# Kernel tuning notes

Hardware: AMD Instinct MI355X
Metric: run time of the kernel (lower is better)

## Reference

```python
import jax, jax.numpy as jnp
import numpy as np

NPOINT = 1024
NSAMPLE = 32
EPS = 1e-5


def setup_inputs() -> dict:
    key = jax.random.key(0)
    ks = jax.random.split(key, 8)
    B, N, D = 16, 4096, 64
    xyz = jax.random.normal(ks[0], (B, N, 3), dtype=jnp.float32)
    points = jax.random.normal(ks[1], (B, N, D), dtype=jnp.float32)

    def mk(k, o, i):
        return (jax.random.normal(k, (o, i), dtype=jnp.float32) * 0.05,
                jnp.zeros((o,), jnp.float32),   # conv bias
                jnp.ones((o,), jnp.float32),    # bn gamma
                jnp.zeros((o,), jnp.float32))   # bn beta

    W0, b0, g0, be0 = mk(ks[2], 64, 67)
    W1, b1, g1, be1 = mk(ks[3], 64, 64)
    W2, b2, g2, be2 = mk(ks[4], 128, 64)
    return dict(xyz=xyz, points=points,
                W0=W0, b0=b0, g0=g0, be0=be0,
                W1=W1, b1=b1, g1=g1, be1=be1,
                W2=W2, b2=b2, g2=g2, be2=be2)


def _fps(xyz, npoint):
    # Sequential farthest point sampling. xyz: [B,N,3] -> idx [B,npoint] int32.
    B, N, _ = xyz.shape
    bidx = jnp.arange(B)

    def step(carry, _):
        distance, farthest = carry
        centroid = xyz[bidx, farthest][:, None, :]          # [B,1,3]
        d = jnp.sum((xyz - centroid) ** 2, -1)              # [B,N]
        distance = jnp.minimum(distance, d)
        new_far = jnp.argmax(distance, -1).astype(jnp.int32)
        return (distance, new_far), farthest

    init = (jnp.full((B, N), jnp.inf, dtype=xyz.dtype),
            jnp.full((B,), N // 2, dtype=jnp.int32))
    _, cents = jax.lax.scan(step, init, None, length=npoint)
    return cents.T                                          # [B, npoint]


def _gather(p, idx):
    # p: [B,N,C], idx: [B,...] -> [B,...,C]
    return jax.vmap(lambda a, i: a[i])(p, idx)


def reference(xyz, points, W0, b0, g0, be0, W1, b1, g1, be1, W2, b2, g2, be2):
    B, N, _ = xyz.shape
    fps_idx = _fps(xyz, NPOINT)                             # [B,M]
    new_xyz = _gather(xyz, fps_idx)                         # [B,M,3]

    # squared distances [B,M,N], then k smallest neighbors
    d = (jnp.sum(new_xyz ** 2, -1)[:, :, None]
         + jnp.sum(xyz ** 2, -1)[:, None, :]
         - 2.0 * jnp.einsum('bmc,bnc->bmn', new_xyz, xyz))
    _, idx = jax.lax.top_k(-d, NSAMPLE)                     # [B,M,K]

    grouped_xyz = _gather(xyz, idx)                         # [B,M,K,3]
    rel = grouped_xyz - new_xyz[:, :, None, :]
    grouped_feat = _gather(points, idx)                     # [B,M,K,D]
    g = jnp.concatenate([rel, grouped_feat], axis=-1)       # [B,M,K,3+D]

    # 1x1 conv + BatchNorm2d (training-mode batch stats) + ReLU
    for W, b, gm, bt in ((W0, b0, g0, be0), (W1, b1, g1, be1), (W2, b2, g2, be2)):
        x = jnp.einsum('bmkc,oc->bmko', g, W) + b
        mu = x.mean((0, 1, 2))
        var = x.var((0, 1, 2))
        g = jax.nn.relu(gm * (x - mu) * jax.lax.rsqrt(var + EPS) + bt)

    new_points = g.max(axis=2)                              # [B,M,C_out]
    return new_xyz, new_points, fps_idx
```

## Files before the change

### kernel.cpp

```cpp
#include <hip/hip_runtime.h>
#include <math.h>

#define B_ 16
#define N_ 4096
#define D_ 64
#define M_ 1024
#define K_ 32
#define RTOT (B_*M_*K_)
#define EPSF 1e-5f

#define WT0B_OFF  0
#define WT1B_OFF  3072
#define WT2B_OFF  5120
#define ST_OFF    9216
#define BN_OFF    9728
#define NXW_OFF   10240
#define KIDX_OFF  59392
#define PK_OFF    583680
#define Y0B_OFF   2680832
#define PTS4_OFF  Y0B_OFF
#define PBF_OFF   19458048
#define SB0_OFF   36235264
#define SB1_OFF   (SB0_OFF + 8192)
#define SB2_OFF   (SB1_OFF + 8192)
#define WS_FAST_BYTES ((unsigned long long)(SB2_OFF + 16384) * 4ull)

typedef __attribute__((ext_vector_type(8))) short bf16x8;
typedef __attribute__((ext_vector_type(4))) float f32x4;

__device__ inline unsigned bf16u(float x) {
    unsigned u = __float_as_uint(x);
    return (u + 0x7FFFu + ((u >> 16) & 1u)) >> 16;
}
__device__ inline float ubf(unsigned short h) {
    return __uint_as_float(((unsigned)h) << 16);
}

#define ROR_MIN(kvar, CTRL) do {                                                   \
    unsigned _lo = (unsigned)(kvar), _hi = (unsigned)((kvar) >> 32);               \
    unsigned _rl = (unsigned)__builtin_amdgcn_update_dpp((int)_lo, (int)_lo, CTRL, 0xF, 0xF, false); \
    unsigned _rh = (unsigned)__builtin_amdgcn_update_dpp((int)_hi, (int)_hi, CTRL, 0xF, 0xF, false); \
    unsigned long long _o = ((unsigned long long)_rh << 32) | _rl;                 \
    if (_o < (kvar)) (kvar) = _o;                                                  \
} while (0)

__global__ void prep_kernel(const float* __restrict__ W0, const float* __restrict__ W1,
                            const float* __restrict__ W2, const float* __restrict__ points,
                            float* __restrict__ ws, int fast) {
    int tid = threadIdx.x;
    int bx = blockIdx.x;
    if (bx >= 17) {
        unsigned short* pbf = (unsigned short*)(ws + PBF_OFF);
        size_t base = (size_t)(bx - 17) * 2048 + (size_t)tid * 8;
        const float4* s = (const float4*)(points + base);
        float4 f0 = s[0], f1 = s[1];
        uint4 u;
        u.x = bf16u(f0.x) | (bf16u(f0.y) << 16);
        u.y = bf16u(f0.z) | (bf16u(f0.w) << 16);
        u.z = bf16u(f1.x) | (bf16u(f1.y) << 16);
        u.w = bf16u(f1.z) | (bf16u(f1.w) << 16);
        *(uint4*)(pbf + base) = u;
        return;
    }
    if (bx > 0) {
        if (fast) {
            float* sb = ws + SB0_OFF + (bx - 1) * 2048;
            for (int i = tid; i < 2048; i += 256) sb[i] = 0.f;
        }
        return;
    }
    unsigned short* wt0b = (unsigned short*)(ws + WT0B_OFF);
    unsigned short* wt1b = (unsigned short*)(ws + WT1B_OFF);
    unsigned short* wt2b = (unsigned short*)(ws + WT2B_OFF);
    float* st = ws + ST_OFF;
    for (int i = tid; i < 512; i += 256) st[i] = 0.f;
    for (int i = tid; i < 64*96; i += 256) {
        int o = i / 96, k = i - o*96;
        float w = 0.f;
        if (k < 64)      w = W0[o*67 + 3 + k];
        else if (k < 67) w = W0[o*67 + (k - 64)];
        wt0b[i] = (unsigned short)bf16u(w);
    }
    for (int i = tid; i < 64*64; i += 256)  wt1b[i] = (unsigned short)bf16u(W1[i]);
    for (int i = tid; i < 128*64; i += 256) wt2b[i] = (unsigned short)bf16u(W2[i]);
}

__global__ __launch_bounds__(256) void fps_kernel(const float* __restrict__ xyz,
                                                  float* __restrict__ out_newxyz,
                                                  float* __restrict__ out_fpsidx,
                                                  float* __restrict__ ws_newxyz,
                                                  float4* __restrict__ pts4g) {
#pragma clang fp contract(off)
    __shared__ float4 pts[N_];
    __shared__ int selidx[M_];
    __shared__ __align__(32) unsigned long long red[2][4];
    const int b = blockIdx.x;
    const int tid = threadIdx.x;
    const int lane = tid & 63, wave = tid >> 6;
    const float* xb = xyz + (size_t)b * N_ * 3;
    for (int i = tid; i < N_; i += 256) {
        float x = xb[i*3+0], y = xb[i*3+1], z = xb[i*3+2];
        pts[i] = make_float4(x, y, z, 0.f);
        if (pts4g) {
            float pp = x*x + y*y; pp = pp + z*z;
            pts4g[b*N_ + i] = make_float4(x, y, z, pp);
        }
    }
    __syncthreads();
    float px[16], py[16], pz[16], dist[16];
#pragma unroll
    for (int j = 0; j < 16; ++j) {
        float4 p = pts[(tid << 4) + j];
        px[j] = p.x; py[j] = p.y; pz[j] = p.z;
        dist[j] = 3.4e38f;
    }
    int cur = N_/2;
    for (int t = 0; t < M_; ++t) {
        if (tid == (t & 255)) selidx[t] = cur;
        if (t == M_-1) break;
        float4 c4 = pts[cur];
        float cx = c4.x, cy = c4.y, cz = c4.z;
        float bm0 = -1.f, bm1 = -1.f, bm2 = -1.f, bm3 = -1.f;
        int bj0 = 0, bj1 = 4, bj2 = 8, bj3 = 12;
#pragma unroll
        for (int j = 0; j < 4; ++j) {
            {
                float dx = px[j]-cx, dy = py[j]-cy, dz = pz[j]-cz;
                float a = dx*dx, b2 = dy*dy, c2 = dz*dz;
                float d = (a + b2) + c2;
                float nd = fminf(dist[j], d); dist[j] = nd;
                bool bt = nd > bm0; bm0 = bt ? nd : bm0; bj0 = bt ? j : bj0;
            }
            {
                int k = j + 4;
                float dx = px[k]-cx, dy = py[k]-cy, dz = pz[k]-cz;
                float a = dx*dx, b2 = dy*dy, c2 = dz*dz;
                float d = (a + b2) + c2;
                float nd = fminf(dist[k], d); dist[k] = nd;
                bool bt = nd > bm1; bm1 = bt ? nd : bm1; bj1 = bt ? k : bj1;
            }
            {
                int k = j + 8;
                float dx = px[k]-cx, dy = py[k]-cy, dz = pz[k]-cz;
                float a = dx*dx, b2 = dy*dy, c2 = dz*dz;
                float d = (a + b2) + c2;
                float nd = fminf(dist[k], d); dist[k] = nd;
                bool bt = nd > bm2; bm2 = bt ? nd : bm2; bj2 = bt ? k : bj2;
            }
            {
                int k = j + 12;
                float dx = px[k]-cx, dy = py[k]-cy, dz = pz[k]-cz;
                float a = dx*dx, b2 = dy*dy, c2 = dz*dz;
                float d = (a + b2) + c2;
                float nd = fminf(dist[k], d); dist[k] = nd;
                bool bt = nd > bm3; bm3 = bt ? nd : bm3; bj3 = bt ? k : bj3;
            }
        }
        float bv = bm0; int bj = bj0;
        if (bm1 > bv) { bv = bm1; bj = bj1; }
        if (bm2 > bv) { bv = bm2; bj = bj2; }
        if (bm3 > bv) { bv = bm3; bj = bj3; }
        unsigned mybits = __float_as_uint(bv);
        unsigned vr = mybits;
        { unsigned o = (unsigned)__builtin_amdgcn_update_dpp((int)vr,(int)vr,0x121,0xF,0xF,false); if (o > vr) vr = o; }
        { unsigned o = (unsigned)__builtin_amdgcn_update_dpp((int)vr,(int)vr,0x122,0xF,0xF,false); if (o > vr) vr = o; }
        { unsigned o = (unsigned)__builtin_amdgcn_update_dpp((int)vr,(int)vr,0x124,0xF,0xF,false); if (o > vr) vr = o; }
        { unsigned o = (unsigned)__builtin_amdgcn_update_dpp((int)vr,(int)vr,0x128,0xF,0xF,false); if (o > vr) vr = o; }
        unsigned r0 = (unsigned)__builtin_amdgcn_readlane((int)vr, 0);
        unsigned r1 = (unsigned)__builtin_amdgcn_readlane((int)vr, 16);
        unsigned r2 = (unsigned)__builtin_amdgcn_readlane((int)vr, 32);
        unsigned r3 = (unsigned)__builtin_amdgcn_readlane((int)vr, 48);
        unsigned m01 = (r0 > r1) ? r0 : r1;
        unsigned m23 = (r2 > r3) ? r2 : r3;
        unsigned vmax = (m01 > m23) ? m01 : m23;
        unsigned long long mask = __ballot(mybits == vmax);
        int wl = (int)__builtin_ctzll(mask);
        int gidx = (tid << 4) + bj;
        int sel = __builtin_amdgcn_readlane(gidx, wl);
        unsigned long long key = ((unsigned long long)vmax << 32) | (unsigned)(~sel);
        int buf = t & 1;
        if (lane == 0) red[buf][wave] = key;
        __syncthreads();
        unsigned long long k0 = red[buf][0], k1 = red[buf][1];
        unsigned long long k2 = red[buf][2], k3 = red[buf][3];
        unsigned long long km01 = (k0 > k1) ? k0 : k1;
        unsigned long long km23 = (k2 > k3) ? k2 : k3;
        unsigned long long km   = (km01 > km23) ? km01 : km23;
        cur = (int)((~(unsigned)km) & (N_-1));
    }
    __syncthreads();
    for (int i = tid; i < M_; i += 256) {
        int c = selidx[i];
        out_fpsidx[b*M_ + i] = (float)c;
        float4 p = pts[c];
        size_t o3 = (size_t)(b*M_ + i)*3;
        out_newxyz[o3+0] = p.x; out_newxyz[o3+1] = p.y; out_newxyz[o3+2] = p.z;
        ws_newxyz[o3+0] = p.x;  ws_newxyz[o3+1] = p.y;  ws_newxyz[o3+2] = p.z;
    }
}

__global__ __launch_bounds__(256) void knn_kernel4(const float4* __restrict__ pts4,
                                                   const float* __restrict__ ws_newxyz,
                                                   int* __restrict__ knn_idx) {
#pragma clang fp contract(off)
    const int lane = threadIdx.x & 63;
    const int q = blockIdx.x * 4 + (threadIdx.x >> 6);
    const int b = q >> 10;
    const float4* pb = pts4 + (size_t)b * N_;
    float qx = ws_newxyz[q*3+0], qy = ws_newxyz[q*3+1], qz = ws_newxyz[q*3+2];
    float qq = qx*qx + qy*qy; qq = qq + qz*qz;
    float val[64];
    float m1 = 3.4e38f, m2 = 3.4e38f; int k1 = 0, k2 = 0;
#pragma unroll
    for (int k = 0; k < 64; ++k) {
        float4 p = pb[(k<<6) + lane];
        float dot = qx*p.x + qy*p.y; dot = dot + qz*p.z;
        float d = (qq + p.w) - 2.0f*dot;
        val[k] = d;
        bool lt1 = d < m1, lt2 = d < m2;
        k2 = lt1 ? k1 : (lt2 ? k : k2);
        m2 = fminf(fmaxf(d, m1), m2);
        k1 = lt1 ? k : k1;
        m1 = fminf(d, m1);
    }
    unsigned long long consumed = 0ull;
    bool has2 = true;
    unsigned int myOut = 0;
    for (int r = 0; r < 32; ++r) {
        unsigned int u = __float_as_uint(m1);
        u = (u & 0x80000000u) ? ~u : (u | 0x80000000u);
        unsigned long long pk = ((unsigned long long)u << 32) | (unsigned)(lane + (k1<<6));
        ROR_MIN(pk, 0x121);
        ROR_MIN(pk, 0x122);
        ROR_MIN(pk, 0x124);
        ROR_MIN(pk, 0x128);
        { unsigned long long o = __shfl_xor(pk, 16); if (o < pk) pk = o; }
        { unsigned long long o = __shfl_xor(pk, 32); if (o < pk) pk = o; }
        unsigned g = (unsigned)pk;
        if (lane == r) myOut = g;
        if (lane == (int)(g & 63u)) {
            consumed |= (1ull << k1);
            if (has2) { m1 = m2; k1 = k2; has2 = false; }
            else {
                m1 = 3.4e38f; k1 = 0;
#pragma unroll
                for (int k = 0; k < 64; ++k) {
                    bool ok = !((consumed >> k) & 1ull) && (val[k] < m1);
                    m1 = ok ? val[k] : m1;
                    k1 = ok ? k : k1;
                }
            }
        }
    }
    if (lane < 32) knn_idx[q*32 + lane] = (int)myOut;
}

__global__ __launch_bounds__(256) void knn_kernel(const float* __restrict__ xyz,
                                                  const float* __restrict__ ws_newxyz,
                                                  int* __restrict__ knn_idx) {
#pragma clang fp contract(off)
    const int lane = threadIdx.x & 63;
    const int q = blockIdx.x * 4 + (threadIdx.x >> 6);
    const int b = q >> 10;
    const float* xb = xyz + (size_t)b * N_ * 3;
    float qx = ws_newxyz[q*3+0], qy = ws_newxyz[q*3+1], qz = ws_newxyz[q*3+2];
    float qq = qx*qx + qy*qy; qq = qq + qz*qz;
    float val[64];
    float m1 = 3.4e38f, m2 = 3.4e38f; int k1 = 0, k2 = 0;
#pragma unroll
    for (int k = 0; k < 64; ++k) {
        int n = (k<<6) + lane;
        float x = xb[n*3+0], y = xb[n*3+1], z = xb[n*3+2];
        float pp = x*x + y*y; pp = pp + z*z;
        float dot = qx*x + qy*y; dot = dot + qz*z;
        float d = (qq + pp) - 2.0f*dot;
        val[k] = d;
        if (d < m1)      { m2 = m1; k2 = k1; m1 = d; k1 = k; }
        else if (d < m2) { m2 = d; k2 = k; }
    }
    unsigned long long consumed = 0ull;
    bool has2 = true;
    unsigned int myOut = 0;
    for (int r = 0; r < 32; ++r) {
        unsigned int u = __float_as_uint(m1);
        u = (u & 0x80000000u) ? ~u : (u | 0x80000000u);
        unsigned long long pk = ((unsigned long long)u << 32) | (unsigned)(lane + (k1<<6));
#pragma unroll
        for (int off = 32; off > 0; off >>= 1) {
            unsigned long long o = __shfl_xor(pk, off);
            pk = (o < pk) ? o : pk;
        }
        unsigned g = (unsigned)pk;
        if (lane == r) myOut = g;
        if (lane == (int)(g & 63u)) {
            consumed |= (1ull << k1);
            if (has2) { m1 = m2; k1 = k2; has2 = false; }
            else {
                m1 = 3.4e38f; k1 = 0;
#pragma unroll
                for (int k = 0; k < 64; ++k) {
                    bool ok = !((consumed >> k) & 1ull) && (val[k] < m1);
                    m1 = ok ? val[k] : m1;
                    k1 = ok ? k : k1;
                }
            }
        }
    }
    if (lane < 32) knn_idx[q*32 + lane] = (int)myOut;
}

__global__ __launch_bounds__(256) void pass0_kernel(
    const float* __restrict__ xyz, const unsigned short* __restrict__ pbf,
    const float* __restrict__ nxw, const int* __restrict__ kidx,
    const unsigned short* __restrict__ wt0b, const float* __restrict__ cb0,
    float* __restrict__ sb,
    unsigned short* __restrict__ y0b)
{
    __shared__ __align__(16) unsigned short XsB[64*104];
    __shared__ __align__(16) unsigned short W0B[64*104];
    __shared__ int sidx[64];
    __shared__ float sAcc[64], qAcc[64];
    const int tid = threadIdx.x;
    const int r0 = blockIdx.x * 64;
    const int lane = tid & 63, wv = tid >> 6;
    const int mrow = lane & 15, quad = lane >> 4;

    if (tid < 64) { sidx[tid] = kidx[r0 + tid]; sAcc[tid] = 0.f; qAcc[tid] = 0.f; }
    {
        const uint4* s = (const uint4*)wt0b;
        for (int i = tid; i < 768; i += 256) {
            int r = i / 12, ch = i - r*12;
            *(uint4*)(W0B + r*104 + ch*8) = s[i];
        }
    }
    __syncthreads();

    {
        int row = tid >> 2, q4 = tid & 3;
        int gr = r0 + row;
        int qq = gr >> 5, bb = qq >> 10;
        int n = sidx[row];
        const uint4* src = (const uint4*)(pbf + ((size_t)(bb*N_ + n))*64 + q4*16);
        *(uint4*)(XsB + row*104 + q4*16)     = src[0];
        *(uint4*)(XsB + row*104 + q4*16 + 8) = src[1];
        uint4 z;
        if (q4 == 0) {
            float rx = xyz[((size_t)(bb*N_ + n))*3 + 0] - nxw[qq*3 + 0];
            float ry = xyz[((size_t)(bb*N_ + n))*3 + 1] - nxw[qq*3 + 1];
            float rz = xyz[((size_t)(bb*N_ + n))*3 + 2] - nxw[qq*3 + 2];
            z.x = bf16u(rx) | (bf16u(ry) << 16);
            z.y = bf16u(rz);
            z.z = 0; z.w = 0;
        } else { z.x = 0; z.y = 0; z.z = 0; z.w = 0; }
        *(uint4*)(XsB + row*104 + 64 + q4*8) = z;
    }
    __syncthreads();

    const int arow = wv*16 + mrow;
    f32x4 acc0[4];
#pragma unroll
    for (int ct = 0; ct < 4; ++ct) {
        float bv = cb0[ct*16 + mrow];
        acc0[ct] = (f32x4){bv, bv, bv, bv};
    }
#pragma unroll
    for (int kk = 0; kk < 96; kk += 32) {
        bf16x8 a = *(const bf16x8*)(XsB + arow*104 + kk + quad*8);
#pragma unroll
        for (int ct = 0; ct < 4; ++ct) {
            bf16x8 b = *(const bf16x8*)(W0B + (ct*16 + mrow)*104 + kk + quad*8);
            acc0[ct] = __builtin_amdgcn_mfma_f32_16x16x32_bf16(a, b, acc0[ct], 0, 0, 0);
        }
    }
#pragma unroll
    for (int ct = 0; ct < 4; ++ct) {
        f32x4 v = acc0[ct];
        float s = (v.x + v.y) + (v.z + v.w);
        float q = (v.x*v.x + v.y*v.y) + (v.z*v.z + v.w*v.w);
        atomicAdd(&sAcc[ct*16 + mrow], s);
        atomicAdd(&qAcc[ct*16 + mrow], q);
    }
    __syncthreads();
    unsigned short* STG = W0B;
    const int rbase = wv*16 + quad*4;
#pragma unroll
    for (int ct = 0; ct < 4; ++ct) {
        int col = ct*16 + mrow;
        f32x4 v = acc0[ct];
        STG[(rbase+0)*72 + col] = (unsigned short)bf16u(v.x);
        STG[(rbase+1)*72 + col] = (unsigned short)bf16u(v.y);
        STG[(rbase+2)*72 + col] = (unsigned short)bf16u(v.z);
        STG[(rbase+3)*72 + col] = (unsigned short)bf16u(v.w);
    }
    __syncthreads();
    for (int i = tid; i < 512; i += 256) {
        int r = i >> 3, c8 = i & 7;
        *(uint4*)(y0b + (size_t)(r0 + r)*64 + c8*8) = *(const uint4*)(STG + r*72 + c8*8);
    }
    int bk = blockIdx.x & 63;
    if (tid < 64) {
        atomicAdd(sb + bk*64 + tid, sAcc[tid]);
        atomicAdd(sb + 4096 + bk*64 + tid, qAcc[tid]);
    }
}

__global__ __launch_bounds__(256) void pass1_kernel(
    const unsigned short* __restrict__ y0b, const unsigned short* __restrict__ wt1b,
    const float* __restrict__ cb1, const float* __restrict__ bnab0,
    float* __restrict__ sb)
{
    __shared__ __align__(16) unsigned short W1B[64*72];
    __shared__ float sAcc[64], qAcc[64];
    const int tid = threadIdx.x;
    const int r0 = blockIdx.x * 64;
    const int lane = tid & 63, wv = tid >> 6;
    const int mrow = lane & 15, quad = lane >> 4;

    {
        const uint4* s = (const uint4*)wt1b;
        for (int i = tid; i < 512; i += 256) {
            int r = i >> 3, ch = i & 7;
            *(uint4*)(W1B + r*72 + ch*8) = s[i];
        }
    }
    if (tid < 64) { sAcc[tid] = 0.f; qAcc[tid] = 0.f; }

    const int gr = r0 + wv*16 + mrow;
    bf16x8 raw0 = *(const bf16x8*)(y0b + (size_t)gr*64 + quad*8);
    bf16x8 raw1 = *(const bf16x8*)(y0b + (size_t)gr*64 + 32 + quad*8);
    bf16x8 a0, a1;
    {
        const float* A = bnab0 + quad*8;
        const float* S = bnab0 + 64 + quad*8;
#pragma unroll
        for (int j = 0; j < 8; ++j) {
            float f = ubf((unsigned short)raw0[j]);
            a0[j] = (short)bf16u(fmaxf(fmaf(A[j], f, S[j]), 0.f));
        }
        const float* A2 = bnab0 + 32 + quad*8;
        const float* S2 = bnab0 + 96 + quad*8;
#pragma unroll
        for (int j = 0; j < 8; ++j) {
            float f = ubf((unsigned short)raw1[j]);
            a1[j] = (short)bf16u(fmaxf(fmaf(A2[j], f, S2[j]), 0.f));
        }
    }
    __syncthreads();

    f32x4 acc[4];
#pragma unroll
    for (int ct = 0; ct < 4; ++ct) {
        float bv = cb1[ct*16 + mrow];
        acc[ct] = (f32x4){bv, bv, bv, bv};
    }
#pragma unroll
    for (int ct = 0; ct < 4; ++ct) {
        bf16x8 b0 = *(const bf16x8*)(W1B + (ct*16 + mrow)*72 + quad*8);
        bf16x8 b1 = *(const bf16x8*)(W1B + (ct*16 + mrow)*72 + 32 + quad*8);
        acc[ct] = __builtin_amdgcn_mfma_f32_16x16x32_bf16(a0, b0, acc[ct], 0, 0, 0);
        acc[ct] = __builtin_amdgcn_mfma_f32_16x16x32_bf16(a1, b1, acc[ct], 0, 0, 0);
    }
#pragma unroll
    for (int ct = 0; ct < 4; ++ct) {
        f32x4 v = acc[ct];
        float s = (v.x + v.y) + (v.z + v.w);
        float q = (v.x*v.x + v.y*v.y) + (v.z*v.z + v.w*v.w);
        atomicAdd(&sAcc[ct*16 + mrow], s);
        atomicAdd(&qAcc[ct*16 + mrow], q);
    }
    __syncthreads();
    int bk = blockIdx.x & 63;
    if (tid < 64) {
        atomicAdd(sb + bk*64 + tid, sAcc[tid]);
        atomicAdd(sb + 4096 + bk*64 + tid, qAcc[tid]);
    }
}

__global__ __launch_bounds__(256) void pass2_kernel(
    const unsigned short* __restrict__ y0b,
    const unsigned short* __restrict__ wt1b, const unsigned short* __restrict__ wt2b,
    const float* __restrict__ cb1, const float* __restrict__ cb2,
    const float* __restrict__ bnab0, const float* __restrict__ bnab1,
    float* __restrict__ sb,
    unsigned int* __restrict__ packed)
{
    __shared__ __align__(16) unsigned short W1B[64*72];
    __shared__ __align__(16) unsigned short W2B[128*72];
    __shared__ __align__(16) unsigned short Gb[64*72];
    __shared__ float sAcc[128], qAcc[128];
    __shared__ float mxs[4*128], mns[4*128];
    const int tid = threadIdx.x;
    const int r0 = blockIdx.x * 64;
    const int lane = tid & 63, wv = tid >> 6;
    const int mrow = lane & 15, quad = lane >> 4;

    {
        const uint4* s = (const uint4*)wt1b;
        for (int i = tid; i < 512; i += 256) {
            int r = i >> 3, ch = i & 7;
            *(uint4*)(W1B + r*72 + ch*8) = s[i];
        }
    }
    {
        const uint4* s = (const uint4*)wt2b;
        for (int i = tid; i < 1024; i += 256) {
            int r = i >> 3, ch = i & 7;
            *(uint4*)(W2B + r*72 + ch*8) = s[i];
        }
    }
    if (tid < 128) { sAcc[tid] = 0.f; qAcc[tid] = 0.f; }

    const int gr = r0 + wv*16 + mrow;
    bf16x8 raw0 = *(const bf16x8*)(y0b + (size_t)gr*64 + quad*8);
    bf16x8 raw1 = *(const bf16x8*)(y0b + (size_t)gr*64 + 32 + quad*8);
    bf16x8 a0, a1;
    {
        const float* A = bnab0 + quad*8;
        const float* S = bnab0 + 64 + quad*8;
#pragma unroll
        for (int j = 0; j < 8; ++j) {
            float f = ubf((unsigned short)raw0[j]);
            a0[j] = (short)bf16u(fmaxf(fmaf(A[j], f, S[j]), 0.f));
        }
        const float* A2 = bnab0 + 32 + quad*8;
        const float* S2 = bnab0 + 96 + quad*8;
#pragma unroll
        for (int j = 0; j < 8; ++j) {
            float f = ubf((unsigned short)raw1[j]);
            a1[j] = (short)bf16u(fmaxf(fmaf(A2[j], f, S2[j]), 0.f));
        }
    }
    __syncthreads();

    f32x4 acc1[4];
#pragma unroll
    for (int ct = 0; ct < 4; ++ct) {
        float bv = cb1[ct*16 + mrow];
        acc1[ct] = (f32x4){bv, bv, bv, bv};
    }
#pragma unroll
    for (int ct = 0; ct < 4; ++ct) {
        bf16x8 b0 = *(const bf16x8*)(W1B + (ct*16 + mrow)*72 + quad*8);
        bf16x8 b1 = *(const bf16x8*)(W1B + (ct*16 + mrow)*72 + 32 + quad*8);
        acc1[ct] = __builtin_amdgcn_mfma_f32_16x16x32_bf16(a0, b0, acc1[ct], 0, 0, 0);
        acc1[ct] = __builtin_amdgcn_mfma_f32_16x16x32_bf16(a1, b1, acc1[ct], 0, 0, 0);
    }
    const int rbase = wv*16 + quad*4;
#pragma unroll
    for (int ct = 0; ct < 4; ++ct) {
        int col = ct*16 + mrow;
        float a = bnab1[col], sh = bnab1[64 + col];
        f32x4 v = acc1[ct];
        Gb[(rbase+0)*72 + col] = (unsigned short)bf16u(fmaxf(fmaf(a, v.x, sh), 0.f));
        Gb[(rbase+1)*72 + col] = (unsigned short)bf16u(fmaxf(fmaf(a, v.y, sh), 0.f));
        Gb[(rbase+2)*72 + col] = (unsigned short)bf16u(fmaxf(fmaf(a, v.z, sh), 0.f));
        Gb[(rbase+3)*72 + col] = (unsigned short)bf16u(fmaxf(fmaf(a, v.w, sh), 0.f));
    }

    const int arow = wv*16 + mrow;
    f32x4 acc[8];
#pragma unroll
    for (int ct = 0; ct < 8; ++ct) {
        float bv = cb2[ct*16 + mrow];
        acc[ct] = (f32x4){bv, bv, bv, bv};
    }
#pragma unroll
    for (int kk = 0; kk < 64; kk += 32) {
        bf16x8 a = *(const bf16x8*)(Gb + arow*72 + kk + quad*8);
#pragma unroll
        for (int ct = 0; ct < 8; ++ct) {
            bf16x8 b = *(const bf16x8*)(W2B + (ct*16 + mrow)*72 + kk + quad*8);
            acc[ct] = __builtin_amdgcn_mfma_f32_16x16x32_bf16(a, b, acc[ct], 0, 0, 0);
        }
    }
#pragma unroll
    for (int ct = 0; ct < 8; ++ct) {
        f32x4 v = acc[ct];
        float s = (v.x + v.y) + (v.z + v.w);
        float q = (v.x*v.x + v.y*v.y) + (v.z*v.z + v.w*v.w);
        atomicAdd(&sAcc[ct*16 + mrow], s);
        atomicAdd(&qAcc[ct*16 + mrow], q);
    }
#pragma unroll
    for (int ct = 0; ct < 8; ++ct) {
        f32x4 v = acc[ct];
        float mx = fmaxf(fmaxf(v.x, v.y), fmaxf(v.z, v.w));
        float mn = fminf(fminf(v.x, v.y), fminf(v.z, v.w));
        { float o = __shfl_xor(mx, 16); mx = fmaxf(mx, o); }
        { float o = __shfl_xor(mn, 16); mn = fminf(mn, o); }
        { float o = __shfl_xor(mx, 32); mx = fmaxf(mx, o); }
        { float o = __shfl_xor(mn, 32); mn = fminf(mn, o); }
        if (quad == 0) {
            mxs[wv*128 + ct*16 + mrow] = mx;
            mns[wv*128 + ct*16 + mrow] = mn;
        }
    }
    __syncthreads();
    {
        int g = tid >> 7, c = tid & 127;
        float mx = fmaxf(mxs[(2*g)*128 + c], mxs[(2*g+1)*128 + c]);
        float mn = fminf(mns[(2*g)*128 + c], mns[(2*g+1)*128 + c]);
        packed[(size_t)(blockIdx.x*2 + g)*128 + c] = (bf16u(mx) << 16) | bf16u(mn);
    }
    int bk = blockIdx.x & 63;
    if (tid < 128) {
        atomicAdd(sb + bk*128 + tid, sAcc[tid]);
        atomicAdd(sb + 8192 + bk*128 + tid, qAcc[tid]);
    }
}

template<int DEPTH>
__global__ __launch_bounds__(256) void mlp_pass(
    const float* __restrict__ xyz, const float* __restrict__ points,
    const float* __restrict__ nxw, const int* __restrict__ kidx,
    const unsigned short* __restrict__ wt0b, const unsigned short* __restrict__ wt1b,
    const unsigned short* __restrict__ wt2b,
    const float* __restrict__ cb0, const float* __restrict__ cb1,
    const float* __restrict__ cb2,
    const float* __restrict__ bnab0, const float* __restrict__ bnab1,
    float* __restrict__ statS, float* __restrict__ statQ,
    unsigned int* __restrict__ packed)
{
    __shared__ __align__(16) unsigned short XsB[64*104];
    __shared__ __align__(16) unsigned short W0B[64*104];
    __shared__ __align__(16) unsigned short W1B[(DEPTH>=2) ? 64*72 : 8];
    __shared__ __align__(16) unsigned short W2B[(DEPTH==3) ? 128*72 : 8];
    __shared__ __align__(16) unsigned short Gb [(DEPTH>=2) ? 64*72 : 8];
    __shared__ float sAcc[128], qAcc[128];
    __shared__ float mxs[(DEPTH==3) ? 4*128 : 1];
    __shared__ float mns[(DEPTH==3) ? 4*128 : 1];

    const int tid = threadIdx.x;
    const int r0 = blockIdx.x * 64;
    const int lane = tid & 63, wv = tid >> 6;
    const int mrow = lane & 15, quad = lane >> 4;

    {
        const uint4* s = (const uint4*)wt0b;
        for (int i = tid; i < 768; i += 256) {
            int r = i / 12, ch = i - r*12;
            *(uint4*)(W0B + r*104 + ch*8) = s[i];
        }
    }
    if constexpr (DEPTH >= 2) {
        const uint4* s = (const uint4*)wt1b;
        for (int i = tid; i < 512; i += 256) {
            int r = i >> 3, ch = i & 7;
            *(uint4*)(W1B + r*72 + ch*8) = s[i];
        }
    }
    if constexpr (DEPTH == 3) {
        const uint4* s = (const uint4*)wt2b;
        for (int i = tid; i < 1024; i += 256) {
            int r = i >> 3, ch = i & 7;
            *(uint4*)(W2B + r*72 + ch*8) = s[i];
        }
    }
    if (tid < 128) { sAcc[tid] = 0.f; qAcc[tid] = 0.f; }

    for (int i = tid; i < 64*96; i += 256) {
        int r = i / 96, c = i - r*96;
        int gr = r0 + r;
        int q = gr >> 5;
        int n = kidx[gr];
        int bb = q >> 10;
        float v = 0.f;
        if (c < 64)      v = points[((size_t)(bb*N_ + n))*64 + c];
        else if (c < 67) v = xyz[((size_t)(bb*N_ + n))*3 + (c-64)] - nxw[q*3 + (c-64)];
        XsB[r*104 + c] = (unsigned short)bf16u(v);
    }
    __syncthreads();

    const int arow = wv*16 + mrow;
    f32x4 acc0[4];
#pragma unroll
    for (int ct = 0; ct < 4; ++ct) {
        float bv = cb0[ct*16 + mrow];
        acc0[ct] = (f32x4){bv, bv, bv, bv};
    }
#pragma unroll
    for (int kk = 0; kk < 96; kk += 32) {
        bf16x8 a = *(const bf16x8*)(XsB + arow*104 + kk + quad*8);
#pragma unroll
        for (int ct = 0; ct < 4; ++ct) {
            bf16x8 b = *(const bf16x8*)(W0B + (ct*16 + mrow)*104 + kk + quad*8);
            acc0[ct] = __builtin_amdgcn_mfma_f32_16x16x32_bf16(a, b, acc0[ct], 0, 0, 0);
        }
    }

    if constexpr (DEPTH == 1) {
// ... 43 lines not shown
                float q = (v.x*v.x + v.y*v.y) + (v.z*v.z + v.w*v.w);
                atomicAdd(&sAcc[ct*16 + mrow], s);
                atomicAdd(&qAcc[ct*16 + mrow], q);
            }
            __syncthreads();
            if (tid < 64) { atomicAdd(statS + tid, sAcc[tid]); atomicAdd(statQ + tid, qAcc[tid]); }
            return;
        } else {
#pragma unroll
            for (int ct = 0; ct < 4; ++ct) {
                int col = ct*16 + mrow;
                float a = bnab1[col], sh = bnab1[64 + col];
                f32x4 v = acc1[ct];
                Gb[(rbase+0)*72 + col] = (unsigned short)bf16u(fmaxf(fmaf(a, v.x, sh), 0.f));
                Gb[(rbase+1)*72 + col] = (unsigned short)bf16u(fmaxf(fmaf(a, v.y, sh), 0.f));
                Gb[(rbase+2)*72 + col] = (unsigned short)bf16u(fmaxf(fmaf(a, v.z, sh), 0.f));
                Gb[(rbase+3)*72 + col] = (unsigned short)bf16u(fmaxf(fmaf(a, v.w, sh), 0.f));
            }
            f32x4 acc2[8];
#pragma unroll
            for (int ct = 0; ct < 8; ++ct) {
                float bv = cb2[ct*16 + mrow];
                acc2[ct] = (f32x4){bv, bv, bv, bv};
            }
#pragma unroll
            for (int kk = 0; kk < 64; kk += 32) {
                bf16x8 a = *(const bf16x8*)(Gb + arow*72 + kk + quad*8);
#pragma unroll
                for (int ct = 0; ct < 8; ++ct) {
                    bf16x8 b = *(const bf16x8*)(W2B + (ct*16 + mrow)*72 + kk + quad*8);
                    acc2[ct] = __builtin_amdgcn_mfma_f32_16x16x32_bf16(a, b, acc2[ct], 0, 0, 0);
                }
            }
#pragma unroll
            for (int ct = 0; ct < 8; ++ct) {
                f32x4 v = acc2[ct];
                float s = (v.x + v.y) + (v.z + v.w);
                float q = (v.x*v.x + v.y*v.y) + (v.z*v.z + v.w*v.w);
                atomicAdd(&sAcc[ct*16 + mrow], s);
                atomicAdd(&qAcc[ct*16 + mrow], q);
            }
#pragma unroll
            for (int ct = 0; ct < 8; ++ct) {
                f32x4 v = acc2[ct];
                float mx = fmaxf(fmaxf(v.x, v.y), fmaxf(v.z, v.w));
                float mn = fminf(fminf(v.x, v.y), fminf(v.z, v.w));
                { float o = __shfl_xor(mx, 16); mx = fmaxf(mx, o); }
                { float o = __shfl_xor(mn, 16); mn = fminf(mn, o); }
                { float o = __shfl_xor(mx, 32); mx = fmaxf(mx, o); }
                { float o = __shfl_xor(mn, 32); mn = fminf(mn, o); }
                if (quad == 0) {
                    mxs[wv*128 + ct*16 + mrow] = mx;
                    mns[wv*128 + ct*16 + mrow] = mn;
                }
            }
            __syncthreads();
            {
                int g = tid >> 7, c = tid & 127;
                float mx = fmaxf(mxs[(2*g)*128 + c], mxs[(2*g+1)*128 + c]);
                float mn = fminf(mns[(2*g)*128 + c], mns[(2*g+1)*128 + c]);
                packed[(size_t)(blockIdx.x*2 + g)*128 + c] = (bf16u(mx) << 16) | bf16u(mn);
            }
            if (tid < 128) { atomicAdd(statS + tid, sAcc[tid]); atomicAdd(statQ + tid, qAcc[tid]); }
        }
    }
}

template<int COUT>
__global__ void bn_finalize(const float* __restrict__ stat_s, const float* __restrict__ stat_q,
                            const float* __restrict__ gamma, const float* __restrict__ beta,
                            float* __restrict__ bnab) {
    int c = threadIdx.x;
    if (c < COUT) {
        const float inv_n = 1.f / (float)RTOT;
        float mu  = stat_s[c] * inv_n;
        float var = stat_q[c] * inv_n - mu*mu;
        float inv = 1.f / sqrtf(var + EPSF);
        float a = gamma[c] * inv;
        bnab[c] = a;
        bnab[COUT + c] = beta[c] - mu * a;
    }
}

template<int COUT>
__global__ __launch_bounds__(256) void bn_finalize_bk(const float* __restrict__ sb,
                               const float* __restrict__ gamma, const float* __restrict__ beta,
                               float* __restrict__ bnab) {
    __shared__ float ps[256], pq[256];
    const int tid = threadIdx.x;
    const int c = tid & (COUT - 1);
    const int g = tid / COUT;
    const int G = 256 / COUT;
    const int per = 64 / G;
    float s = 0.f, q = 0.f;
    for (int k = g*per; k < (g+1)*per; ++k) {
        s += sb[k*COUT + c];
        q += sb[64*COUT + k*COUT + c];
    }
    ps[tid] = s; pq[tid] = q;
    __syncthreads();
    if (tid < COUT) {
        for (int g2 = 1; g2 < G; ++g2) { s += ps[g2*COUT + tid]; q += pq[g2*COUT + tid]; }
        const float inv_n = 1.f / (float)RTOT;
        float mu  = s * inv_n;
        float var = q * inv_n - mu*mu;
        float inv = 1.f / sqrtf(var + EPSF);
        float a = gamma[tid] * inv;
        bnab[tid] = a;
        bnab[COUT + tid] = beta[tid] - mu * a;
    }
}

__global__ __launch_bounds__(256) void final_out(const unsigned int* __restrict__ packed,
                                                 const float* __restrict__ bnab2,
                                                 float* __restrict__ out_np) {
    int idx = blockIdx.x*256 + threadIdx.x;
    int c = idx & 127;
    float a = bnab2[c], sh = bnab2[128 + c];
    unsigned p = packed[idx];
    float mx = __uint_as_float(p & 0xFFFF0000u);
    float mn = __uint_as_float(p << 16);
    float x = (a >= 0.f) ? mx : mn;
    out_np[idx] = fmaxf(fmaf(a, x, sh), 0.f);
}

extern "C" void kernel_launch(void* const* d_in, const int* in_sizes, int n_in,
                              void* d_out, int out_size, void* d_ws, size_t ws_size,
                              hipStream_t stream) {
    const float* xyz    = (const float*)d_in[0];
    const float* points = (const float*)d_in[1];
    const float* W0 = (const float*)d_in[2];
    const float* b0 = (const float*)d_in[3];
    const float* g0 = (const float*)d_in[4];
    const float* be0= (const float*)d_in[5];
    const float* W1 = (const float*)d_in[6];
    const float* b1 = (const float*)d_in[7];
    const float* g1 = (const float*)d_in[8];
    const float* be1= (const float*)d_in[9];
    const float* W2 = (const float*)d_in[10];
    const float* b2 = (const float*)d_in[11];
    const float* g2 = (const float*)d_in[12];
    const float* be2= (const float*)d_in[13];

    float* ws  = (float*)d_ws;
    float* out = (float*)d_out;
    float* out_newxyz = out;
    float* out_np     = out + 49152;
    float* out_fpsidx = out + 49152 + 2097152;

    unsigned short* wt0b = (unsigned short*)(ws + WT0B_OFF);
    unsigned short* wt1b = (unsigned short*)(ws + WT1B_OFF);
    unsigned short* wt2b = (unsigned short*)(ws + WT2B_OFF);
    float* s0 = ws + ST_OFF;        float* q0 = s0 + 64;
    float* s1 = q0 + 64;            float* q1 = s1 + 64;
    float* s2 = q1 + 64;            float* q2 = s2 + 128;
    float* bnab0 = ws + BN_OFF;     float* bnab1 = bnab0 + 128;  float* bnab2 = bnab1 + 128;
    float* nxw   = ws + NXW_OFF;
    int*   kidx  = (int*)(ws + KIDX_OFF);
    unsigned int* packed = (unsigned int*)(ws + PK_OFF);
    unsigned short* y0b = (unsigned short*)(ws + Y0B_OFF);
    unsigned short* pbf = (unsigned short*)(ws + PBF_OFF);
    float4* pts4 = (float4*)(ws + PTS4_OFF);
    float* sb0 = ws + SB0_OFF;
    float* sb1 = ws + SB1_OFF;
    float* sb2 = ws + SB2_OFF;

    int fast = (ws_size >= WS_FAST_BYTES) ? 1 : 0;

    prep_kernel<<<fast ? (17 + 2048) : 17, 256, 0, stream>>>(W0, W1, W2, points, ws, fast);
    fps_kernel<<<B_, 256, 0, stream>>>(xyz, out_newxyz, out_fpsidx, nxw,
                                       fast ? pts4 : nullptr);
    if (fast)
        knn_kernel4<<<(B_*M_)/4, 256, 0, stream>>>(pts4, nxw, kidx);
    else
        knn_kernel<<<(B_*M_)/4, 256, 0, stream>>>(xyz, nxw, kidx);

    if (fast) {
        pass0_kernel<<<RTOT/64, 256, 0, stream>>>(xyz, pbf, nxw, kidx, wt0b, b0, sb0, y0b);
        bn_finalize_bk<64><<<1, 256, 0, stream>>>(sb0, g0, be0, bnab0);
        pass1_kernel<<<RTOT/64, 256, 0, stream>>>(y0b, wt1b, b1, bnab0, sb1);
        bn_finalize_bk<64><<<1, 256, 0, stream>>>(sb1, g1, be1, bnab1);
        pass2_kernel<<<RTOT/64, 256, 0, stream>>>(y0b, wt1b, wt2b, b1, b2, bnab0, bnab1, sb2, packed);
        bn_finalize_bk<128><<<1, 256, 0, stream>>>(sb2, g2, be2, bnab2);
    } else {
        mlp_pass<1><<<RTOT/64, 256, 0, stream>>>(xyz, points, nxw, kidx, wt0b, wt1b, wt2b,
            b0, b1, b2, nullptr, nullptr, s0, q0, nullptr);
        bn_finalize<64><<<1, 64, 0, stream>>>(s0, q0, g0, be0, bnab0);
        mlp_pass<2><<<RTOT/64, 256, 0, stream>>>(xyz, points, nxw, kidx, wt0b, wt1b, wt2b,
            b0, b1, b2, bnab0, nullptr, s1, q1, nullptr);
        bn_finalize<64><<<1, 64, 0, stream>>>(s1, q1, g1, be1, bnab1);
        mlp_pass<3><<<RTOT/64, 256, 0, stream>>>(xyz, points, nxw, kidx, wt0b, wt1b, wt2b,
            b0, b1, b2, bnab0, bnab1, s2, q2, packed);
        bn_finalize<128><<<1, 128, 0, stream>>>(s2, q2, g2, be2, bnab2);
    }

    final_out<<<(B_*M_*128)/256, 256, 0, stream>>>(packed, bnab2, out_np);
}
```

Before: 1.309 ms.

## Fuse prep into FPS, KNN into pass0, BN finalize into consumers

Weight conversion, points-to-bf16 conversion and stats zeroing move into extra blocks of the FPS launch, so they run alongside the sequential FPS blocks. The KNN top-k is computed inside pass0 by two waves per block while the other two load weights, which removes the separate KNN kernel and its index round trip. Each BN finalize now runs redundantly inside every pass1/pass2 block and in a fused final output kernel. This cuts the fast path from ten launches to five, at the cost of every block re-reducing the per-bucket stat sums and of fewer waves per block doing the KNN work.

```diff
diff --git a/kernel.cpp b/kernel.cpp
--- a/kernel.cpp
+++ b/kernel.cpp
@@ -44,14 +44,25 @@
     if (_o < (kvar)) (kvar) = _o;                                                  \
 } while (0)
 
-__global__ void prep_kernel(const float* __restrict__ W0, const float* __restrict__ W1,
-                            const float* __restrict__ W2, const float* __restrict__ points,
-                            float* __restrict__ ws, int fast) {
-    int tid = threadIdx.x;
-    int bx = blockIdx.x;
-    if (bx >= 17) {
+__global__ __launch_bounds__(256) void fps_kernel(const float* __restrict__ xyz,
+                                                  float* __restrict__ out_newxyz,
+                                                  float* __restrict__ out_fpsidx,
+                                                  float* __restrict__ ws_newxyz,
+                                                  float4* __restrict__ pts4g,
+                                                  const float* __restrict__ W0,
+                                                  const float* __restrict__ W1,
+                                                  const float* __restrict__ W2,
+                                                  const float* __restrict__ points,
+                                                  float* __restrict__ ws, int fast) {
+#pragma clang fp contract(off)
+    __shared__ float4 pts[N_];
+    __shared__ int selidx[M_];
+    __shared__ __align__(32) unsigned long long red[2][4];
+    const int bx = blockIdx.x;
+    const int tid = threadIdx.x;
+    if (bx >= 33) {
         unsigned short* pbf = (unsigned short*)(ws + PBF_OFF);
-        size_t base = (size_t)(bx - 17) * 2048 + (size_t)tid * 8;
+        size_t base = (size_t)(bx - 33) * 2048 + (size_t)tid * 8;
         const float4* s = (const float4*)(points + base);
         float4 f0 = s[0], f1 = s[1];
         uint4 u;
@@ -62,40 +73,31 @@
         *(uint4*)(pbf + base) = u;
         return;
     }
-    if (bx > 0) {
+    if (bx >= 17) {
         if (fast) {
-            float* sb = ws + SB0_OFF + (bx - 1) * 2048;
+            float* sb = ws + SB0_OFF + (bx - 17) * 2048;
             for (int i = tid; i < 2048; i += 256) sb[i] = 0.f;
         }
         return;
     }
-    unsigned short* wt0b = (unsigned short*)(ws + WT0B_OFF);
-    unsigned short* wt1b = (unsigned short*)(ws + WT1B_OFF);
-    unsigned short* wt2b = (unsigned short*)(ws + WT2B_OFF);
-    float* st = ws + ST_OFF;
-    for (int i = tid; i < 512; i += 256) st[i] = 0.f;
-    for (int i = tid; i < 64*96; i += 256) {
-        int o = i / 96, k = i - o*96;
-        float w = 0.f;
-        if (k < 64)      w = W0[o*67 + 3 + k];
-        else if (k < 67) w = W0[o*67 + (k - 64)];
-        wt0b[i] = (unsigned short)bf16u(w);
-    }
-    for (int i = tid; i < 64*64; i += 256)  wt1b[i] = (unsigned short)bf16u(W1[i]);
-    for (int i = tid; i < 128*64; i += 256) wt2b[i] = (unsigned short)bf16u(W2[i]);
-}
-
-__global__ __launch_bounds__(256) void fps_kernel(const float* __restrict__ xyz,
-                                                  float* __restrict__ out_newxyz,
-                                                  float* __restrict__ out_fpsidx,
-                                                  float* __restrict__ ws_newxyz,
-                                                  float4* __restrict__ pts4g) {
-#pragma clang fp contract(off)
-    __shared__ float4 pts[N_];
-    __shared__ int selidx[M_];
-    __shared__ __align__(32) unsigned long long red[2][4];
-    const int b = blockIdx.x;
-    const int tid = threadIdx.x;
+    if (bx == 16) {
+        unsigned short* wt0b = (unsigned short*)(ws + WT0B_OFF);
+        unsigned short* wt1b = (unsigned short*)(ws + WT1B_OFF);
+        unsigned short* wt2b = (unsigned short*)(ws + WT2B_OFF);
+        float* st = ws + ST_OFF;
+        for (int i = tid; i < 512; i += 256) st[i] = 0.f;
+        for (int i = tid; i < 64*96; i += 256) {
+            int o = i / 96, k = i - o*96;
+            float w = 0.f;
+            if (k < 64)      w = W0[o*67 + 3 + k];
+            else if (k < 67) w = W0[o*67 + (k - 64)];
+            wt0b[i] = (unsigned short)bf16u(w);
+        }
+        for (int i = tid; i < 64*64; i += 256)  wt1b[i] = (unsigned short)bf16u(W1[i]);
+        for (int i = tid; i < 128*64; i += 256) wt2b[i] = (unsigned short)bf16u(W2[i]);
+        return;
+    }
+    const int b = bx;
     const int lane = tid & 63, wave = tid >> 6;
     const float* xb = xyz + (size_t)b * N_ * 3;
     for (int i = tid; i < N_; i += 256) {
@@ -199,62 +201,6 @@
     }
 }
 
-__global__ __launch_bounds__(256) void knn_kernel4(const float4* __restrict__ pts4,
-                                                   const float* __restrict__ ws_newxyz,
-                                                   int* __restrict__ knn_idx) {
-#pragma clang fp contract(off)
-    const int lane = threadIdx.x & 63;
-    const int q = blockIdx.x * 4 + (threadIdx.x >> 6);
-    const int b = q >> 10;
-    const float4* pb = pts4 + (size_t)b * N_;
-    float qx = ws_newxyz[q*3+0], qy = ws_newxyz[q*3+1], qz = ws_newxyz[q*3+2];
-    float qq = qx*qx + qy*qy; qq = qq + qz*qz;
-    float val[64];
-    float m1 = 3.4e38f, m2 = 3.4e38f; int k1 = 0, k2 = 0;
-#pragma unroll
-    for (int k = 0; k < 64; ++k) {
-        float4 p = pb[(k<<6) + lane];
-        float dot = qx*p.x + qy*p.y; dot = dot + qz*p.z;
-        float d = (qq + p.w) - 2.0f*dot;
-        val[k] = d;
-        bool lt1 = d < m1, lt2 = d < m2;
-        k2 = lt1 ? k1 : (lt2 ? k : k2);
-        m2 = fminf(fmaxf(d, m1), m2);
-        k1 = lt1 ? k : k1;
-        m1 = fminf(d, m1);
-    }
-    unsigned long long consumed = 0ull;
-    bool has2 = true;
-    unsigned int myOut = 0;
-    for (int r = 0; r < 32; ++r) {
-        unsigned int u = __float_as_uint(m1);
-        u = (u & 0x80000000u) ? ~u : (u | 0x80000000u);
-        unsigned long long pk = ((unsigned long long)u << 32) | (unsigned)(lane + (k1<<6));
-        ROR_MIN(pk, 0x121);
-        ROR_MIN(pk, 0x122);
-        ROR_MIN(pk, 0x124);
-        ROR_MIN(pk, 0x128);
-        { unsigned long long o = __shfl_xor(pk, 16); if (o < pk) pk = o; }
-        { unsigned long long o = __shfl_xor(pk, 32); if (o < pk) pk = o; }
-        unsigned g = (unsigned)pk;
-        if (lane == r) myOut = g;
-        if (lane == (int)(g & 63u)) {
-            consumed |= (1ull << k1);
-            if (has2) { m1 = m2; k1 = k2; has2 = false; }
-            else {
-                m1 = 3.4e38f; k1 = 0;
-#pragma unroll
-                for (int k = 0; k < 64; ++k) {
-                    bool ok = !((consumed >> k) & 1ull) && (val[k] < m1);
-                    m1 = ok ? val[k] : m1;
-                    k1 = ok ? k : k1;
-                }
-            }
-        }
-    }
-    if (lane < 32) knn_idx[q*32 + lane] = (int)myOut;
-}
-
 __global__ __launch_bounds__(256) void knn_kernel(const float* __restrict__ xyz,
                                                   const float* __restrict__ ws_newxyz,
                                                   int* __restrict__ knn_idx) {
@@ -311,11 +257,12 @@
 
 __global__ __launch_bounds__(256) void pass0_kernel(
     const float* __restrict__ xyz, const unsigned short* __restrict__ pbf,
-    const float* __restrict__ nxw, const int* __restrict__ kidx,
+    const float* __restrict__ nxw, const float4* __restrict__ pts4,
     const unsigned short* __restrict__ wt0b, const float* __restrict__ cb0,
     float* __restrict__ sb,
     unsigned short* __restrict__ y0b)
 {
+#pragma clang fp contract(off)
     __shared__ __align__(16) unsigned short XsB[64*104];
     __shared__ __align__(16) unsigned short W0B[64*104];
     __shared__ int sidx[64];
@@ -325,13 +272,63 @@
     const int lane = tid & 63, wv = tid >> 6;
     const int mrow = lane & 15, quad = lane >> 4;
 
-    if (tid < 64) { sidx[tid] = kidx[r0 + tid]; sAcc[tid] = 0.f; qAcc[tid] = 0.f; }
-    {
+    if (tid < 64) { sAcc[tid] = 0.f; qAcc[tid] = 0.f; }
+    if (wv >= 2) {
         const uint4* s = (const uint4*)wt0b;
-        for (int i = tid; i < 768; i += 256) {
+        for (int i = tid - 128; i < 768; i += 128) {
             int r = i / 12, ch = i - r*12;
             *(uint4*)(W0B + r*104 + ch*8) = s[i];
         }
+    } else {
+        const int q = blockIdx.x * 2 + wv;
+        const int b = q >> 10;
+        const float4* pb = pts4 + (size_t)b * N_;
+        float qx = nxw[q*3+0], qy = nxw[q*3+1], qz = nxw[q*3+2];
+        float qq = qx*qx + qy*qy; qq = qq + qz*qz;
+        float val[64];
+        float m1 = 3.4e38f, m2 = 3.4e38f; int k1 = 0, k2 = 0;
+#pragma unroll
+        for (int k = 0; k < 64; ++k) {
+            float4 p = pb[(k<<6) + lane];
+            float dot = qx*p.x + qy*p.y; dot = dot + qz*p.z;
+            float d = (qq + p.w) - 2.0f*dot;
+            val[k] = d;
+            bool lt1 = d < m1, lt2 = d < m2;
+            k2 = lt1 ? k1 : (lt2 ? k : k2);
+            m2 = fminf(fmaxf(d, m1), m2);
+            k1 = lt1 ? k : k1;
+            m1 = fminf(d, m1);
+        }
+        unsigned long long consumed = 0ull;
+        bool has2 = true;
+        unsigned int myOut = 0;
+        for (int r = 0; r < 32; ++r) {
+            unsigned int u = __float_as_uint(m1);
+            u = (u & 0x80000000u) ? ~u : (u | 0x80000000u);
+            unsigned long long pk = ((unsigned long long)u << 32) | (unsigned)(lane + (k1<<6));
+            ROR_MIN(pk, 0x121);
+            ROR_MIN(pk, 0x122);
+            ROR_MIN(pk, 0x124);
+            ROR_MIN(pk, 0x128);
+            { unsigned long long o = __shfl_xor(pk, 16); if (o < pk) pk = o; }
+            { unsigned long long o = __shfl_xor(pk, 32); if (o < pk) pk = o; }
+            unsigned g = (unsigned)pk;
+            if (lane == r) myOut = g;
+            if (lane == (int)(g & 63u)) {
+                consumed |= (1ull << k1);
+                if (has2) { m1 = m2; k1 = k2; has2 = false; }
+                else {
+                    m1 = 3.4e38f; k1 = 0;
+#pragma unroll
+                    for (int k = 0; k < 64; ++k) {
+                        bool ok = !((consumed >> k) & 1ull) && (val[k] < m1);
+                        m1 = ok ? val[k] : m1;
+                        k1 = ok ? k : k1;
+                    }
+                }
+            }
+        }
+        if (lane < 32) sidx[wv*32 + lane] = (int)myOut;
     }
     __syncthreads();
 
@@ -404,12 +401,42 @@
     }
 }
 
+__device__ inline void bn64_block(const float* __restrict__ sb,
+                                  const float* __restrict__ gamma,
+                                  const float* __restrict__ beta,
+                                  float* __restrict__ ps, float* __restrict__ pq,
+                                  float* __restrict__ bnabL, int tid) {
+    const int c = tid & 63;
+    const int g = tid >> 6;
+    float s = 0.f, q = 0.f;
+    for (int k = g*16; k < (g+1)*16; ++k) {
+        s += sb[k*64 + c];
+        q += sb[4096 + k*64 + c];
+    }
+    ps[tid] = s; pq[tid] = q;
+    __syncthreads();
+    if (tid < 64) {
+        for (int g2 = 1; g2 < 4; ++g2) { s += ps[g2*64 + tid]; q += pq[g2*64 + tid]; }
+        const float inv_n = 1.f / (float)RTOT;
+        float mu  = s * inv_n;
+        float var = q * inv_n - mu*mu;
+        float inv = 1.f / sqrtf(var + EPSF);
+        float a = gamma[tid] * inv;
+        bnabL[tid] = a;
+        bnabL[64 + tid] = beta[tid] - mu * a;
+    }
+    __syncthreads();
+}
+
 __global__ __launch_bounds__(256) void pass1_kernel(
     const unsigned short* __restrict__ y0b, const unsigned short* __restrict__ wt1b,
-    const float* __restrict__ cb1, const float* __restrict__ bnab0,
-    float* __restrict__ sb)
+    const float* __restrict__ cb1,
+    const float* __restrict__ g0, const float* __restrict__ be0,
+    const float* __restrict__ sb0, float* __restrict__ sb1)
 {
     __shared__ __align__(16) unsigned short W1B[64*72];
+    __shared__ float ps[256], pq[256];
+    __shared__ float bnab0L[128];
     __shared__ float sAcc[64], qAcc[64];
     const int tid = threadIdx.x;
     const int r0 = blockIdx.x * 64;
@@ -424,28 +451,28 @@
         }
     }
     if (tid < 64) { sAcc[tid] = 0.f; qAcc[tid] = 0.f; }
+    bn64_block(sb0, g0, be0, ps, pq, bnab0L, tid);
 
     const int gr = r0 + wv*16 + mrow;
     bf16x8 raw0 = *(const bf16x8*)(y0b + (size_t)gr*64 + quad*8);
     bf16x8 raw1 = *(const bf16x8*)(y0b + (size_t)gr*64 + 32 + quad*8);
     bf16x8 a0, a1;
     {
-        const float* A = bnab0 + quad*8;
-        const float* S = bnab0 + 64 + quad*8;
+        const float* A = bnab0L + quad*8;
+        const float* S = bnab0L + 64 + quad*8;
 #pragma unroll
         for (int j = 0; j < 8; ++j) {
             float f = ubf((unsigned short)raw0[j]);
             a0[j] = (short)bf16u(fmaxf(fmaf(A[j], f, S[j]), 0.f));
         }
-        const float* A2 = bnab0 + 32 + quad*8;
-        const float* S2 = bnab0 + 96 + quad*8;
+        const float* A2 = bnab0L + 32 + quad*8;
+        const float* S2 = bnab0L + 96 + quad*8;
 #pragma unroll
         for (int j = 0; j < 8; ++j) {
             float f = ubf((unsigned short)raw1[j]);
             a1[j] = (short)bf16u(fmaxf(fmaf(A2[j], f, S2[j]), 0.f));
         }
     }
-    __syncthreads();
 
     f32x4 acc[4];
 #pragma unroll
@@ -471,8 +498,8 @@
     __syncthreads();
     int bk = blockIdx.x & 63;
     if (tid < 64) {
-        atomicAdd(sb + bk*64 + tid, sAcc[tid]);
-        atomicAdd(sb + 4096 + bk*64 + tid, qAcc[tid]);
+        atomicAdd(sb1 + bk*64 + tid, sAcc[tid]);
+        atomicAdd(sb1 + 4096 + bk*64 + tid, qAcc[tid]);
     }
 }
 
@@ -480,13 +507,17 @@
     const unsigned short* __restrict__ y0b,
     const unsigned short* __restrict__ wt1b, const unsigned short* __restrict__ wt2b,
     const float* __restrict__ cb1, const float* __restrict__ cb2,
-    const float* __restrict__ bnab0, const float* __restrict__ bnab1,
-    float* __restrict__ sb,
+    const float* __restrict__ g0, const float* __restrict__ be0,
+    const float* __restrict__ g1, const float* __restrict__ be1,
+    const float* __restrict__ sb0, const float* __restrict__ sb1,
+    float* __restrict__ sb2,
     unsigned int* __restrict__ packed)
 {
     __shared__ __align__(16) unsigned short W1B[64*72];
     __shared__ __align__(16) unsigned short W2B[128*72];
     __shared__ __align__(16) unsigned short Gb[64*72];
+    __shared__ float ps[256], pq[256];
+    __shared__ float bnab0L[128], bnab1L[128];
     __shared__ float sAcc[128], qAcc[128];
     __shared__ float mxs[4*128], mns[4*128];
     const int tid = threadIdx.x;
@@ -509,28 +540,29 @@
         }
     }
     if (tid < 128) { sAcc[tid] = 0.f; qAcc[tid] = 0.f; }
+    bn64_block(sb0, g0, be0, ps, pq, bnab0L, tid);
+    bn64_block(sb1, g1, be1, ps, pq, bnab1L, tid);
 
     const int gr = r0 + wv*16 + mrow;
     bf16x8 raw0 = *(const bf16x8*)(y0b + (size_t)gr*64 + quad*8);
     bf16x8 raw1 = *(const bf16x8*)(y0b + (size_t)gr*64 + 32 + quad*8);
     bf16x8 a0, a1;
     {
-        const float* A = bnab0 + quad*8;
-        const float* S = bnab0 + 64 + quad*8;
+        const float* A = bnab0L + quad*8;
+        const float* S = bnab0L + 64 + quad*8;
 #pragma unroll
         for (int j = 0; j < 8; ++j) {
             float f = ubf((unsigned short)raw0[j]);
             a0[j] = (short)bf16u(fmaxf(fmaf(A[j], f, S[j]), 0.f));
         }
-        const float* A2 = bnab0 + 32 + quad*8;
-        const float* S2 = bnab0 + 96 + quad*8;
+        const float* A2 = bnab0L + 32 + quad*8;
+        const float* S2 = bnab0L + 96 + quad*8;
 #pragma unroll
         for (int j = 0; j < 8; ++j) {
             float f = ubf((unsigned short)raw1[j]);
             a1[j] = (short)bf16u(fmaxf(fmaf(A2[j], f, S2[j]), 0.f));
         }
     }
-    __syncthreads();
 
     f32x4 acc1[4];
 #pragma unroll
@@ -549,7 +581,7 @@
 #pragma unroll
     for (int ct = 0; ct < 4; ++ct) {
         int col = ct*16 + mrow;
-        float a = bnab1[col], sh = bnab1[64 + col];
+        float a = bnab1L[col], sh = bnab1L[64 + col];
         f32x4 v = acc1[ct];
         Gb[(rbase+0)*72 + col] = (unsigned short)bf16u(fmaxf(fmaf(a, v.x, sh), 0.f));
         Gb[(rbase+1)*72 + col] = (unsigned short)bf16u(fmaxf(fmaf(a, v.y, sh), 0.f));
@@ -604,8 +636,50 @@
     }
     int bk = blockIdx.x & 63;
     if (tid < 128) {
-        atomicAdd(sb + bk*128 + tid, sAcc[tid]);
-        atomicAdd(sb + 8192 + bk*128 + tid, qAcc[tid]);
+        atomicAdd(sb2 + bk*128 + tid, sAcc[tid]);
+        atomicAdd(sb2 + 8192 + bk*128 + tid, qAcc[tid]);
+    }
+}
+
+__global__ __launch_bounds__(256) void final_fast(const unsigned int* __restrict__ packed,
+                                                  const float* __restrict__ sb2,
+                                                  const float* __restrict__ g2,
+                                                  const float* __restrict__ be2,
+                                                  float* __restrict__ out_np) {
+    __shared__ float ps[256], pq[256];
+    __shared__ float bn[256];
+    const int tid = threadIdx.x;
+    const int c = tid & 127;
+    const int g = tid >> 7;
+    float s = 0.f, q = 0.f;
+    for (int k = g*32; k < (g+1)*32; ++k) {
+        s += sb2[k*128 + c];
+        q += sb2[8192 + k*128 + c];
+    }
+    ps[tid] = s; pq[tid] = q;
+    __syncthreads();
+    if (tid < 128) {
+        s += ps[128 + tid]; q += pq[128 + tid];
+        const float inv_n = 1.f / (float)RTOT;
+        float mu  = s * inv_n;
+        float var = q * inv_n - mu*mu;
+        float inv = 1.f / sqrtf(var + EPSF);
+        float a = g2[tid] * inv;
+        bn[tid] = a;
+        bn[128 + tid] = be2[tid] - mu * a;
+    }
+    __syncthreads();
+    const size_t base = (size_t)blockIdx.x * 8192;
+#pragma unroll 4
+    for (int j = 0; j < 32; ++j) {
+        size_t idx = base + j*256 + tid;
+        int cc = (int)(idx & 127);
+        float a = bn[cc], sh = bn[128 + cc];
+        unsigned p = packed[idx];
+        float mx = __uint_as_float(p & 0xFFFF0000u);
+        float mn = __uint_as_float(p << 16);
+        float x = (a >= 0.f) ? mx : mn;
+        out_np[idx] = fmaxf(fmaf(a, x, sh), 0.f);
     }
 }
 
@@ -815,35 +889,6 @@
     }
 }
 
-template<int COUT>
-__global__ __launch_bounds__(256) void bn_finalize_bk(const float* __restrict__ sb,
-                               const float* __restrict__ gamma, const float* __restrict__ beta,
-                               float* __restrict__ bnab) {
-    __shared__ float ps[256], pq[256];
-    const int tid = threadIdx.x;
-    const int c = tid & (COUT - 1);
-    const int g = tid / COUT;
-    const int G = 256 / COUT;
-    const int per = 64 / G;
-    float s = 0.f, q = 0.f;
-    for (int k = g*per; k < (g+1)*per; ++k) {
-        s += sb[k*COUT + c];
-        q += sb[64*COUT + k*COUT + c];
-    }
-    ps[tid] = s; pq[tid] = q;
-    __syncthreads();
-    if (tid < COUT) {
-        for (int g2 = 1; g2 < G; ++g2) { s += ps[g2*COUT + tid]; q += pq[g2*COUT + tid]; }
-        const float inv_n = 1.f / (float)RTOT;
-        float mu  = s * inv_n;
-        float var = q * inv_n - mu*mu;
-        float inv = 1.f / sqrtf(var + EPSF);
-        float a = gamma[tid] * inv;
-        bnab[tid] = a;
-        bnab[COUT + tid] = beta[tid] - mu * a;
-    }
-}
-
 __global__ __launch_bounds__(256) void final_out(const unsigned int* __restrict__ packed,
                                                  const float* __restrict__ bnab2,
                                                  float* __restrict__ out_np) {
@@ -900,22 +945,17 @@
 
     int fast = (ws_size >= WS_FAST_BYTES) ? 1 : 0;
 
-    prep_kernel<<<fast ? (17 + 2048) : 17, 256, 0, stream>>>(W0, W1, W2, points, ws, fast);
-    fps_kernel<<<B_, 256, 0, stream>>>(xyz, out_newxyz, out_fpsidx, nxw,
-                                       fast ? pts4 : nullptr);
-    if (fast)
-        knn_kernel4<<<(B_*M_)/4, 256, 0, stream>>>(pts4, nxw, kidx);
-    else
+    fps_kernel<<<fast ? 2081 : 17, 256, 0, stream>>>(xyz, out_newxyz, out_fpsidx, nxw,
+        fast ? pts4 : nullptr, W0, W1, W2, points, ws, fast);
+
+    if (fast) {
+        pass0_kernel<<<RTOT/64, 256, 0, stream>>>(xyz, pbf, nxw, pts4, wt0b, b0, sb0, y0b);
+        pass1_kernel<<<RTOT/64, 256, 0, stream>>>(y0b, wt1b, b1, g0, be0, sb0, sb1);
+        pass2_kernel<<<RTOT/64, 256, 0, stream>>>(y0b, wt1b, wt2b, b1, b2,
+                                                  g0, be0, g1, be1, sb0, sb1, sb2, packed);
+        final_fast<<<256, 256, 0, stream>>>(packed, sb2, g2, be2, out_np);
+    } else {
         knn_kernel<<<(B_*M_)/4, 256, 0, stream>>>(xyz, nxw, kidx);
-
-    if (fast) {
-        pass0_kernel<<<RTOT/64, 256, 0, stream>>>(xyz, pbf, nxw, kidx, wt0b, b0, sb0, y0b);
-        bn_finalize_bk<64><<<1, 256, 0, stream>>>(sb0, g0, be0, bnab0);
-        pass1_kernel<<<RTOT/64, 256, 0, stream>>>(y0b, wt1b, b1, bnab0, sb1);
-        bn_finalize_bk<64><<<1, 256, 0, stream>>>(sb1, g1, be1, bnab1);
-        pass2_kernel<<<RTOT/64, 256, 0, stream>>>(y0b, wt1b, wt2b, b1, b2, bnab0, bnab1, sb2, packed);
-        bn_finalize_bk<128><<<1, 256, 0, stream>>>(sb2, g2, be2, bnab2);
-    } else {
         mlp_pass<1><<<RTOT/64, 256, 0, stream>>>(xyz, points, nxw, kidx, wt0b, wt1b, wt2b,
             b0, b1, b2, nullptr, nullptr, s0, q0, nullptr);
         bn_finalize<64><<<1, 64, 0, stream>>>(s0, q0, g0, be0, bnab0);
@@ -925,7 +965,6 @@
         mlp_pass<3><<<RTOT/64, 256, 0, stream>>>(xyz, points, nxw, kidx, wt0b, wt1b, wt2b,
             b0, b1, b2, bnab0, bnab1, s2, q2, packed);
         bn_finalize<128><<<1, 128, 0, stream>>>(s2, q2, g2, be2, bnab2);
-    }
-
-    final_out<<<(B_*M_*128)/256, 256, 0, stream>>>(packed, bnab2, out_np);
-}
+        final_out<<<(B_*M_*128)/256, 256, 0, stream>>>(packed, bnab2, out_np);
+    }
+}
```

Result: no change. 1.323 ms (+1.0%).
